# Kernel tuning notes

Measured on AMD Instinct MI355X. Metric: run time of the kernel, lower is better.

The kernel has to match this reference:

```python
import jax, jax.numpy as jnp
import numpy as np

N, E, D = 50000, 800000, 128
RESIDUAL_SCALE = 1.0
EPS = 1e-5  # torch LayerNorm default eps


def _mlp_ln(h, w1, b1, w2, b2, w3, b3, g, beta):
    # MeshGraphNets MLP: Linear -> SiLU -> Linear -> SiLU -> Linear -> LayerNorm
    h = jax.nn.silu(h @ w1 + b1)
    h = jax.nn.silu(h @ w2 + b2)
    h = h @ w3 + b3
    mu = h.mean(axis=-1, keepdims=True)
    var = ((h - mu) ** 2).mean(axis=-1, keepdims=True)
    return g * (h - mu) * jax.lax.rsqrt(var + EPS) + beta


def setup_inputs() -> dict:
    key = jax.random.key(0)
    ks = jax.random.split(key, 16)

    def lin(k, fan_in, fan_out):
        bound = 1.0 / np.sqrt(fan_in)
        kw, kb = jax.random.split(k)
        w = jax.random.uniform(kw, (fan_in, fan_out), jnp.float32, -bound, bound)
        b = jax.random.uniform(kb, (fan_out,), jnp.float32, -bound, bound)
        return w, b

    x = jax.random.normal(ks[0], (N, D), jnp.float32)
    edge_attr = jax.random.normal(ks[1], (E, D), jnp.float32)
    edge_index = jax.random.randint(ks[2], (2, E), 0, N, jnp.int32)

    ew1, eb1 = lin(ks[3], 3 * D, D)
    ew2, eb2 = lin(ks[4], D, D)
    ew3, eb3 = lin(ks[5], D, D)
    e_gamma = jnp.ones((D,), jnp.float32)
    e_beta = jnp.zeros((D,), jnp.float32)

    nw1, nb1 = lin(ks[6], 2 * D, D)
    nw2, nb2 = lin(ks[7], D, D)
    nw3, nb3 = lin(ks[8], D, D)
    n_gamma = jnp.ones((D,), jnp.float32)
    n_beta = jnp.zeros((D,), jnp.float32)

    return dict(x=x, edge_attr=edge_attr, edge_index=edge_index,
                ew1=ew1, eb1=eb1, ew2=ew2, eb2=eb2, ew3=ew3, eb3=eb3,
                e_gamma=e_gamma, e_beta=e_beta,
                nw1=nw1, nb1=nb1, nw2=nw2, nb2=nb2, nw3=nw3, nb3=nb3,
                n_gamma=n_gamma, n_beta=n_beta)


def reference(x, edge_attr, edge_index,
              ew1, eb1, ew2, eb2, ew3, eb3, e_gamma, e_beta,
              nw1, nb1, nw2, nb2, nw3, nb3, n_gamma, n_beta):
    senders, receivers = edge_index[0], edge_index[1]

    # EdgeBlock: gather endpoint node features, concat with edge_attr, MLP
    edge_in = jnp.concatenate([x[senders], x[receivers], edge_attr], axis=-1)  # [E, 3D]
    edge_mlp_out = _mlp_ln(edge_in, ew1, eb1, ew2, eb2, ew3, eb3, e_gamma, e_beta)  # [E, D]

    # NodeBlock: scatter-sum edge messages to receiver nodes, concat with x, MLP
    agg = jax.ops.segment_sum(edge_mlp_out, receivers, num_segments=N)  # [N, D]
    node_in = jnp.concatenate([x, agg], axis=-1)  # [N, 2D]
    node_mlp_out = _mlp_ln(node_in, nw1, nb1, nw2, nb2, nw3, nb3, n_gamma, n_beta)

    # Residual updates
    x_new = x + RESIDUAL_SCALE * node_mlp_out

    # PairNorm (use_pairnorm=True)
    x_centered = x_new - x_new.mean(axis=0, keepdims=True)
    rms = jnp.linalg.norm(x_centered) / jnp.sqrt(jnp.float32(x_new.shape[0])) + 1e-8
    x_new = x_centered / rms

    edge_attr_new = edge_attr + RESIDUAL_SCALE * edge_mlp_out
    return x_new, edge_attr_new
```

## Files before the change

### kernel.cpp

```cpp
#include <hip/hip_runtime.h>
#include <hip/hip_bf16.h>

#define NN 50000
#define NE 800000
#define ROWB 272

typedef unsigned short u16;
typedef unsigned int u32;
typedef __attribute__((ext_vector_type(4))) float f32x4;
typedef __attribute__((ext_vector_type(8))) short short8;


__device__ __forceinline__ u16 f2b(float f){ __hip_bfloat16 h = __float2bfloat16(f); u16 u; __builtin_memcpy(&u, &h, 2); return u; }
__device__ __forceinline__ float b2f(u16 u){ __hip_bfloat16 h; __builtin_memcpy(&h, &u, 2); return __bfloat162float(h); }
__device__ __forceinline__ float siluf(float v){
  const float e = __expf(-v);
  return v * __builtin_amdgcn_rcpf(1.f + e);
}

__device__ __forceinline__ uint4 cvt8(const float* __restrict__ s){
  const float4 a = *(const float4*)s;
  const float4 b = *(const float4*)(s + 4);
  union { u16 h[8]; uint4 q; } u;
  u.h[0]=f2b(a.x); u.h[1]=f2b(a.y); u.h[2]=f2b(a.z); u.h[3]=f2b(a.w);
  u.h[4]=f2b(b.x); u.h[5]=f2b(b.y); u.h[6]=f2b(b.z); u.h[7]=f2b(b.w);
  return u.q;
}

template<int K>
__device__ __forceinline__ void gemm128(f32x4 acc[4][2], const u16* __restrict__ sA,
                                        const u16* __restrict__ wB, int wm, int wn, int lane){
  const int l15 = lane & 15, l4 = lane >> 4;
  const u16* w0 = wB + (size_t)(wn*32 + l15)*K + l4*8;
  const u16* w1 = w0 + (size_t)16*K;
  #pragma unroll
  for (int ks = 0; ks < 4; ++ks){
    const short8 b0 = *(const short8*)(w0 + ks*32);
    const short8 b1 = *(const short8*)(w1 + ks*32);
    const int kb = ks*64 + l4*16;
    short8 a[4];
    #pragma unroll
    for (int fr = 0; fr < 4; ++fr)
      a[fr] = *(const short8*)((const char*)sA + (wm*64 + fr*16 + l15)*ROWB + kb);
    #pragma unroll
    for (int fr = 0; fr < 4; ++fr){
      acc[fr][0] = __builtin_amdgcn_mfma_f32_16x16x32_bf16(a[fr], b0, acc[fr][0], 0, 0, 0);
      acc[fr][1] = __builtin_amdgcn_mfma_f32_16x16x32_bf16(a[fr], b1, acc[fr][1], 0, 0, 0);
    }
  }
}

template<int K>
__device__ __forceinline__ void gemm64(f32x4 acc[2][4], const u16* __restrict__ sA,
                                       const u16* __restrict__ wB, int wm, int wn, int lane){
  const int l15 = lane & 15, l4 = lane >> 4;
  const u16* w0 = wB + (size_t)(wn*64 + l15)*K + l4*8;
  #pragma unroll
  for (int ks = 0; ks < 4; ++ks){
    short8 b[4];
    #pragma unroll
    for (int fc = 0; fc < 4; ++fc)
      b[fc] = *(const short8*)(w0 + (size_t)fc*16*K + ks*32);
    const int kb = ks*64 + l4*16;
    short8 a[2];
    #pragma unroll
    for (int fr = 0; fr < 2; ++fr)
      a[fr] = *(const short8*)((const char*)sA + (wm*32 + fr*16 + l15)*ROWB + kb);
    #pragma unroll
    for (int fr = 0; fr < 2; ++fr)
      #pragma unroll
      for (int fc = 0; fc < 4; ++fc)
        acc[fr][fc] = __builtin_amdgcn_mfma_f32_16x16x32_bf16(a[fr], b[fc], acc[fr][fc], 0, 0, 0);
  }
}

__device__ __forceinline__ void epilogue(const f32x4 acc[4][2], const float* __restrict__ bias,
                                         u16* __restrict__ dst, int wm, int wn, int lane, bool doSilu){
  const int l15 = lane & 15, l4 = lane >> 4;
  #pragma unroll
  for (int fc = 0; fc < 2; ++fc){
    const int col = wn*32 + fc*16 + l15;
    const float bv = bias[col];
    #pragma unroll
    for (int fr = 0; fr < 4; ++fr){
      const int rbase = wm*64 + fr*16 + l4*4;
      #pragma unroll
      for (int j = 0; j < 4; ++j){
        float v = acc[fr][fc][j] + bv;
        if (doSilu) v = siluf(v);
        *(u16*)((char*)dst + (rbase + j)*ROWB + col*2) = f2b(v);
      }
    }
  }
}

__device__ __forceinline__ void epilogue64(const f32x4 acc[2][4], const float* __restrict__ bias,
                                           u16* __restrict__ dst, int wm, int wn, int lane, bool doSilu){
  const int l15 = lane & 15, l4 = lane >> 4;
  #pragma unroll
  for (int fc = 0; fc < 4; ++fc){
    const int col = wn*64 + fc*16 + l15;
    const float bv = bias[col];
    #pragma unroll
    for (int fr = 0; fr < 2; ++fr){
      const int rbase = wm*32 + fr*16 + l4*4;
      #pragma unroll
      for (int j = 0; j < 4; ++j){
        float v = acc[fr][fc][j] + bv;
        if (doSilu) v = siluf(v);
        *(u16*)((char*)dst + (rbase + j)*ROWB + col*2) = f2b(v);
      }
    }
  }
}

__global__ __launch_bounds__(256) void prep_kernel(const float* __restrict__ w1, const float* __restrict__ w2,
                                                   const float* __restrict__ w3, const float* __restrict__ m1,
                                                   const float* __restrict__ m2, const float* __restrict__ m3,
                                                   u16* __restrict__ wt,
                                                   const float* __restrict__ x, u16* __restrict__ xB,
                                                   const int* __restrict__ eidx, int* __restrict__ cnt){
  const int i = blockIdx.x * 256 + threadIdx.x;
  if (i < 147456){
    const float* src; int K, base, off;
    if      (i < 49152)  { src = w1; K = 384; base = 0;      off = i; }
    else if (i < 65536)  { src = w2; K = 128; base = 49152;  off = i - 49152; }
    else if (i < 81920)  { src = w3; K = 128; base = 65536;  off = i - 65536; }
    else if (i < 114688) { src = m1; K = 256; base = 81920;  off = i - 81920; }
    else if (i < 131072) { src = m2; K = 128; base = 114688; off = i - 114688; }
    else                 { src = m3; K = 128; base = 131072; off = i - 131072; }
    const int k = off >> 7, n = off & 127;
    wt[base + n*K + k] = f2b(src[off]);
  }
  if (xB){
    const size_t o = (size_t)i * 8;
    *(uint4*)(xB + o) = cvt8(x + o);
  }
  atomicAdd(&cnt[eidx[NE + i]], 1);
}

__global__ __launch_bounds__(256) void scatter_kernel(const int* __restrict__ eidx, int* __restrict__ cursor,
                                                      int* __restrict__ perm){
  const int i = blockIdx.x * 256 + threadIdx.x;
  if (i < NE){
    const int pos = atomicAdd(&cursor[eidx[NE + i]], 1);
    perm[pos] = i;
  }
}

__global__ __launch_bounds__(256, 4) void scanpre_kernel(const int* __restrict__ cnt, int* __restrict__ off,
                                                         int* __restrict__ cursor,
                                                         const float* __restrict__ x, const u16* __restrict__ xB,
                                                         const u16* __restrict__ wt, u16* __restrict__ Pab){
  const int t = threadIdx.x;
  if (blockIdx.x == 0){
    __shared__ int s[256];
    const int CH = 196;
    int sum = 0;
    for (int i = 0; i < CH; ++i){
      const int idx = t*CH + i;
      if (idx < NN) sum += cnt[idx];
    }
    s[t] = sum;
    __syncthreads();
    for (int d = 1; d < 256; d <<= 1){
      int v = (t >= d) ? s[t - d] : 0;
      __syncthreads();
      s[t] += v;
      __syncthreads();
    }
    int run = s[t] - sum;
    for (int i = 0; i < CH; ++i){
      const int idx = t*CH + i;
      if (idx < NN){
        off[idx] = run;
        cursor[idx] = run;
        run += cnt[idx];
        if (idx == NN - 1) off[NN] = run;
      }
    }
    return;
  }

  __shared__ u16 sX[64*136];
  const int nBase = (blockIdx.x - 1) * 64;
  const int lane = t & 63, wid = t >> 6;
  const int wm = wid >> 1, wn = wid & 1;
  const int chunk = t & 15, r0 = t >> 4;

  #pragma unroll
  for (int p = 0; p < 4; ++p){
    const int row = r0 + p*16;
    const int node = nBase + row;
    uint4 v = {0u, 0u, 0u, 0u};
    if (node < NN){
      if (xB) v = *(const uint4*)(xB + (size_t)node*128 + chunk*8);
      else    v = cvt8(x + (size_t)node*128 + chunk*8);
    }
    *(uint4*)((char*)sX + row*ROWB + chunk*16) = v;
  }
  __syncthreads();

  const f32x4 z4 = {0.f, 0.f, 0.f, 0.f};
  const int l15 = lane & 15, l4 = lane >> 4;
  #pragma unroll
  for (int half = 0; half < 2; ++half){
    f32x4 acc[2][4];
    #pragma unroll
    for (int fr = 0; fr < 2; ++fr)
      #pragma unroll
      for (int fc = 0; fc < 4; ++fc) acc[fr][fc] = z4;
    gemm64<384>(acc, sX, wt + half*128, wm, wn, lane);
    #pragma unroll
    for (int fc = 0; fc < 4; ++fc){
      const int col = wn*64 + fc*16 + l15;
      #pragma unroll
      for (int fr = 0; fr < 2; ++fr){
        const int rbase = wm*32 + fr*16 + l4*4;
        #pragma unroll
        for (int j = 0; j < 4; ++j){
          const int node = nBase + rbase + j;
          if (node < NN) Pab[(size_t)node*256 + half*128 + col] = f2b(acc[fr][fc][j]);
        }
      }
    }
  }
}

__global__ __launch_bounds__(512, 4) void edge_kernel(
    const float* __restrict__ ea, const int* __restrict__ eidx,
    const u16* __restrict__ wt, const u16* __restrict__ Pab,
    const float* __restrict__ b1, const float* __restrict__ b2,
    const float* __restrict__ b3, const float* __restrict__ gma, const float* __restrict__ bta,
    int* __restrict__ cursor, float* __restrict__ outE, u16* __restrict__ oBuf)
{
  __shared__ u16 sA[128*136];
  __shared__ float sMeta[640];
  __shared__ int sIdx[256];
  __shared__ int sSlot[128];
  const int t = threadIdx.x;
  const size_t eBase = (size_t)blockIdx.x * 128;

  if (t < 128){
    sIdx[t] = eidx[eBase + t];
    const int r = eidx[(size_t)NE + eBase + t];
    sIdx[t + 128] = r;
    if (oBuf) sSlot[t] = atomicAdd(&cursor[r], 1);
    sMeta[t]       = b1[t];
    sMeta[t + 128] = b2[t];
    sMeta[t + 256] = b3[t];
    sMeta[t + 384] = gma[t];
    sMeta[t + 512] = bta[t];
  }
  __syncthreads();

  const int lane = t & 63, wid = t >> 6;
  const int wm = wid >> 2, wn = wid & 3;
  const int chunk = t & 15, r0 = t >> 4;
  const int l15 = lane & 15, l4 = lane >> 4;

  uint4 eaQ[4];
  #pragma unroll
  for (int p = 0; p < 4; ++p){
    const int row = r0 + p*32;
    uint4 v = cvt8(ea + ((eBase + row)*128 + chunk*8));
    eaQ[p] = v;
    *(uint4*)((char*)sA + row*ROWB + chunk*16) = v;
  }

  f32x4 acc[4][2];
  #pragma unroll
  for (int fr = 0; fr < 4; ++fr){
    #pragma unroll
    for (int j = 0; j < 4; ++j){
      const int row = wm*64 + fr*16 + l4*4 + j;
      const u16* pa = Pab + (size_t)sIdx[row]*256;
      const u16* pb = Pab + (size_t)sIdx[row + 128]*256 + 128;
      #pragma unroll
      for (int fc = 0; fc < 2; ++fc){
        const int col = wn*32 + fc*16 + l15;
        acc[fr][fc][j] = b2f(pa[col]) + b2f(pb[col]);
      }
    }
  }
  __syncthreads();

  gemm128<384>(acc, sA, wt + 256, wm, wn, lane);
  __syncthreads();
  epilogue(acc, sMeta + 0, sA, wm, wn, lane, true);
  __syncthreads();
  const f32x4 z4 = {0.f, 0.f, 0.f, 0.f};
  #pragma unroll
  for (int fr = 0; fr < 4; ++fr){ acc[fr][0] = z4; acc[fr][1] = z4; }
  gemm128<128>(acc, sA, wt + 49152, wm, wn, lane);
  __syncthreads();
  epilogue(acc, sMeta + 128, sA, wm, wn, lane, true);
  __syncthreads();
  #pragma unroll
  for (int fr = 0; fr < 4; ++fr){ acc[fr][0] = z4; acc[fr][1] = z4; }
  gemm128<128>(acc, sA, wt + 65536, wm, wn, lane);
  __syncthreads();
  epilogue(acc, sMeta + 256, sA, wm, wn, lane, false);
  __syncthreads();

  {
    #pragma unroll
    for (int p = 0; p < 4; ++p){
      const int row = r0 + p*32;
      uint4 q = *(const uint4*)((const char*)sA + row*ROWB + chunk*16);
      const u16* pu = (const u16*)&q;
      float h[8];
      #pragma unroll
      for (int j = 0; j < 8; ++j) h[j] = b2f(pu[j]);
      float s = 0.f;
      #pragma unroll
      for (int j = 0; j < 8; ++j) s += h[j];
      s += __shfl_xor(s, 1); s += __shfl_xor(s, 2); s += __shfl_xor(s, 4); s += __shfl_xor(s, 8);
      const float mu = s * (1.f/128.f);
      float ss = 0.f;
      #pragma unroll
      for (int j = 0; j < 8; ++j){ const float d = h[j] - mu; ss += d*d; }
      ss += __shfl_xor(ss, 1); ss += __shfl_xor(ss, 2); ss += __shfl_xor(ss, 4); ss += __shfl_xor(ss, 8);
      const float rs = rsqrtf(fmaxf(ss*(1.f/128.f), 0.f) + 1e-5f);
      const size_t e = eBase + row;
      const u16* ep = (const u16*)&eaQ[p];
      alignas(16) float orow[8];
      alignas(16) u16 obf[8];
      #pragma unroll
      for (int j = 0; j < 8; ++j){
        const int col = chunk*8 + j;
        const float o = sMeta[384 + col]*(h[j] - mu)*rs + sMeta[512 + col];
        orow[j] = b2f(ep[j]) + o;
        obf[j] = f2b(o);
      }
      float* dst = outE + e*128 + chunk*8;
      *(float4*)dst       = ((const float4*)orow)[0];
      *(float4*)(dst + 4) = ((const float4*)orow)[1];
      if (oBuf) *(uint4*)(oBuf + (size_t)sSlot[row]*128 + chunk*8) = *(const uint4*)obf;
    }
  }
}

__global__ __launch_bounds__(256) void agg_f_kernel(const float* __restrict__ outE, const float* __restrict__ ea,
                                                    const int* __restrict__ off, const int* __restrict__ perm,
                                                    float* __restrict__ agg){
  const int node = blockIdx.x * 4 + (threadIdx.x >> 6);
  const int lane = threadIdx.x & 63;
  if (node >= NN) return;
  const int s = off[node], e = off[node + 1];
  float a0 = 0.f, a1 = 0.f;
  for (int i = s; i < e; ++i){
    const size_t r = (size_t)perm[i] * 128;
    a0 += outE[r + lane]      - ea[r + lane];
    a1 += outE[r + 64 + lane] - ea[r + 64 + lane];
  }
  agg[(size_t)node*128 + lane]      = a0;
  agg[(size_t)node*128 + 64 + lane] = a1;
}

__global__ __launch_bounds__(256, 4) void node_kernel(
    const float* __restrict__ x, const float* __restrict__ aggF,
    const u16* __restrict__ oBuf, const int* __restrict__ off,
    const u16* __restrict__ wt,
    const float* __restrict__ b1, const float* __restrict__ b2, const float* __restrict__ b3,
    const float* __restrict__ gma, const float* __restrict__ bta,
    float* __restrict__ outX, float* __restrict__ stats)
{
  __shared__ u16 sA[64*136];
  __shared__ float sMeta[640];
  __shared__ float sCol[128];
  __shared__ float sSq;
  const int t = threadIdx.x;
  const int nBase = blockIdx.x * 64;

  if (t < 128){
    sMeta[t]       = b1[t];
    sMeta[t + 128] = b2[t];
    sMeta[t + 256] = b3[t];
    sMeta[t + 384] = gma[t];
    sMeta[t + 512] = bta[t];
    sCol[t] = 0.f;
  }
  if (t == 0) sSq = 0.f;
  __syncthreads();

  const int lane = t & 63, wid = t >> 6;
  const int wm = wid >> 1, wn = wid & 1;
  const int chunk = t & 15, r0 = t >> 4;

  const f32x4 z4 = {0.f, 0.f, 0.f, 0.f};
  f32x4 acc[2][4];
  #pragma unroll
  for (int fr = 0; fr < 2; ++fr)
    #pragma unroll
    for (int fc = 0; fc < 4; ++fc) acc[fr][fc] = z4;

  for (int kc = 0; kc < 2; ++kc){
    #pragma unroll
    for (int p = 0; p < 4; ++p){
      const int row = r0 + p*16;
      const int node = nBase + row;
      uint4 v = {0u, 0u, 0u, 0u};
      if (node < NN){
        if (kc == 0){
          v = cvt8(x + (size_t)node*128 + chunk*8);
        } else if (oBuf){
          float a[8] = {0.f,0.f,0.f,0.f,0.f,0.f,0.f,0.f};
          const int s0 = off[node], e0 = off[node + 1];
          for (int i = s0; i < e0; ++i){
            uint4 q = *(const uint4*)(oBuf + (size_t)i*128 + chunk*8);
            const u16* pu = (const u16*)&q;
            #pragma unroll
            for (int j = 0; j < 8; ++j) a[j] += b2f(pu[j]);
          }
          union { u16 h[8]; uint4 q; } u;
          #pragma unroll
          for (int j = 0; j < 8; ++j) u.h[j] = f2b(a[j]);
          v = u.q;
        } else {
          v = cvt8(aggF + (size_t)node*128 + chunk*8);
        }
      }
      *(uint4*)((char*)sA + row*ROWB + chunk*16) = v;
    }
    __syncthreads();
    gemm64<256>(acc, sA, wt + 81920 + kc*128, wm, wn, lane);
    __syncthreads();
  }
  epilogue64(acc, sMeta + 0, sA, wm, wn, lane, true);
  __syncthreads();
  #pragma unroll
  for (int fr = 0; fr < 2; ++fr)
    #pragma unroll
    for (int fc = 0; fc < 4; ++fc) acc[fr][fc] = z4;
  gemm64<128>(acc, sA, wt + 114688, wm, wn, lane);
  __syncthreads();
  epilogue64(acc, sMeta + 128, sA, wm, wn, lane, true);
  __syncthreads();
  #pragma unroll
  for (int fr = 0; fr < 2; ++fr)
    #pragma unroll
    for (int fc = 0; fc < 4; ++fc) acc[fr][fc] = z4;
  gemm64<128>(acc, sA, wt + 131072, wm, wn, lane);
  __syncthreads();
  epilogue64(acc, sMeta + 256, sA, wm, wn, lane, false);
  __syncthreads();

  {
    float lssq = 0.f;
    #pragma unroll
    for (int p = 0; p < 4; ++p){
      const int row = r0 + p*16;
      const int node = nBase + row;
      uint4 q = *(const uint4*)((const char*)sA + row*ROWB + chunk*16);
      const u16* pu = (const u16*)&q;
      float h[8];
      #pragma unroll
      for (int j = 0; j < 8; ++j) h[j] = b2f(pu[j]);
      float s = 0.f;
      #pragma unroll
      for (int j = 0; j < 8; ++j) s += h[j];
      s += __shfl_xor(s, 1); s += __shfl_xor(s, 2); s += __shfl_xor(s, 4); s += __shfl_xor(s, 8);
      const float mu = s * (1.f/128.f);
      float ss = 0.f;
      #pragma unroll
      for (int j = 0; j < 8; ++j){ const float d = h[j] - mu; ss += d*d; }
      ss += __shfl_xor(ss, 1); ss += __shfl_xor(ss, 2); ss += __shfl_xor(ss, 4); ss += __shfl_xor(ss, 8);
      const float rs = rsqrtf(fmaxf(ss*(1.f/128.f), 0.f) + 1e-5f);
      if (node < NN){
        const float* xRow = x + (size_t)node*128 + chunk*8;
        const float4 xa = *(const float4*)xRow;
        const float4 xb = *(const float4*)(xRow + 4);
        float xr[8] = {xa.x, xa.y, xa.z, xa.w, xb.x, xb.y, xb.z, xb.w};
        alignas(16) float orow[8];
        #pragma unroll
        for (int j = 0; j < 8; ++j){
          const int col = chunk*8 + j;
          const float o = sMeta[384 + col]*(h[j] - mu)*rs + sMeta[512 + col];
          const float res = xr[j] + o;
          orow[j] = res;
          atomicAdd(&sCol[col], res);
          lssq += res*res;
        }
        float* dst = outX + (size_t)node*128 + chunk*8;
        *(float4*)dst       = ((const float4*)orow)[0];
        *(float4*)(dst + 4) = ((const float4*)orow)[1];
      }
    }
    #pragma unroll
    for (int m = 1; m < 64; m <<= 1) lssq += __shfl_xor(lssq, m);
    if (lane == 0) atomicAdd(&sSq, lssq);
  }
  __syncthreads();
  if (t < 128) atomicAdd(&stats[t], sCol[t]);
  if (t == 0)  atomicAdd(&stats[128], sSq);
}

__global__ __launch_bounds__(256) void pairnorm_kernel(float* __restrict__ xOut, const float* __restrict__ stats){
  __shared__ float sMean[128];
  __shared__ float sP2[2];
  __shared__ float sInv;
  const int t = threadIdx.x;
  float m2 = 0.f;
  if (t < 128){
    const float mean = stats[t] * (1.f / (float)NN);
    sMean[t] = mean;
    m2 = mean * mean;
  }
  #pragma unroll
  for (int m = 1; m < 64; m <<= 1) m2 += __shfl_xor(m2, m);
  if ((t & 63) == 0 && t < 128) sP2[t >> 6] = m2;
  __syncthreads();
  if (t == 0){
    float ssc = stats[128] - (float)NN * (sP2[0] + sP2[1]);
    ssc = fmaxf(ssc, 0.f);
    const float rms = sqrtf(ssc * (1.f / (float)NN)) + 1e-8f;
    sInv = 1.f / rms;
  }
  __syncthreads();
  const size_t base = ((size_t)blockIdx.x * 256 + t) * 4;
  const int col = (int)(base & 127);
  float4 q = *(float4*)(xOut + base);
  const float inv = sInv;
  q.x = (q.x - sMean[col])     * inv;
  q.y = (q.y - sMean[col + 1]) * inv;
  q.z = (q.z - sMean[col + 2]) * inv;
  q.w = (q.w - sMean[col + 3]) * inv;
  *(float4*)(xOut + base) = q;
}

extern "C" void kernel_launch(void* const* d_in, const int* in_sizes, int n_in,
                              void* d_out, int out_size, void* d_ws, size_t ws_size,
                              hipStream_t stream){
  (void)in_sizes; (void)n_in; (void)out_size;
  const float* x    = (const float*)d_in[0];
  const float* ea   = (const float*)d_in[1];
  const int*   eidx = (const int*)d_in[2];
  const float* ew1  = (const float*)d_in[3];
  const float* eb1  = (const float*)d_in[4];
  const float* ew2  = (const float*)d_in[5];
  const float* eb2  = (const float*)d_in[6];
  const float* ew3  = (const float*)d_in[7];
  const float* eb3  = (const float*)d_in[8];
  const float* eg   = (const float*)d_in[9];
  const float* ebt  = (const float*)d_in[10];
  const float* nw1  = (const float*)d_in[11];
  const float* nb1  = (const float*)d_in[12];
  const float* nw2  = (const float*)d_in[13];
  const float* nb2  = (const float*)d_in[14];
  const float* nw3  = (const float*)d_in[15];
  const float* nb3  = (const float*)d_in[16];
  const float* ng   = (const float*)d_in[17];
  const float* nbt  = (const float*)d_in[18];

  u16*   wt     = (u16*)d_ws;
  float* stats  = (float*)((char*)d_ws + 294912);
  int*   cnt    = (int*)((char*)d_ws + 297216);
  int*   off    = (int*)((char*)d_ws + 497408);
  int*   cursor = (int*)((char*)d_ws + 697600);
  int*   perm   = (int*)((char*)d_ws + 897792);
  const bool useO = ws_size >= (7297792ull + (size_t)NE * 128 * 2);
  const bool useX = ws_size >= (7297792ull + (size_t)NE * 128 * 2 + (size_t)NN * 128 * 2);
  u16*   oBuf   = useO ? (u16*)((char*)d_ws + 7297792) : (u16*)nullptr;
  u16*   xB     = useX ? (u16*)((char*)d_ws + 7297792 + (size_t)NE * 128 * 2) : (u16*)nullptr;
  float* outX   = (float*)d_out;
  u16*   Pab    = (u16*)d_out;
  float* outE   = outX + (size_t)NN * 128;

  hipMemsetAsync((char*)d_ws + 294912, 0, 202496, stream);
  prep_kernel<<<3125, 256, 0, stream>>>(ew1, ew2, ew3, nw1, nw2, nw3, wt, x, xB, eidx, cnt);
  scanpre_kernel<<<783, 256, 0, stream>>>(cnt, off, cursor, x, xB, wt, Pab);
  if (!useO) scatter_kernel<<<3125, 256, 0, stream>>>(eidx, cursor, perm);
  edge_kernel<<<6250, 512, 0, stream>>>(ea, eidx, wt, Pab, eb1, eb2, eb3, eg, ebt, cursor, outE, oBuf);
  if (!useO) agg_f_kernel<<<12500, 256, 0, stream>>>(outE, ea, off, perm, outX);
  node_kernel<<<782, 256, 0, stream>>>(x, outX, oBuf, off, wt, nb1, nb2, nb3, ng, nbt, outX, stats);
  pairnorm_kernel<<<6250, 256, 0, stream>>>(outX, stats);
}
```

Before: 685.4 us.

## Give each wave its own 16-row band to drop block syncs in MLP kernels

Result: slower. 1.245 ms (+81.7%).

```diff
diff --git a/kernel.cpp b/kernel.cpp
--- a/kernel.cpp
+++ b/kernel.cpp
@@ -4,6 +4,7 @@
 #define NN 50000
 #define NE 800000
 #define ROWB 272
+#define NROWB 528
 
 typedef unsigned short u16;
 typedef unsigned int u32;
@@ -27,25 +28,31 @@
   return u.q;
 }
 
-template<int K>
-__device__ __forceinline__ void gemm128(f32x4 acc[4][2], const u16* __restrict__ sA,
-                                        const u16* __restrict__ wB, int wm, int wn, int lane){
-  const int l15 = lane & 15, l4 = lane >> 4;
-  const u16* w0 = wB + (size_t)(wn*32 + l15)*K + l4*8;
-  const u16* w1 = w0 + (size_t)16*K;
+template<int Kw>
+__device__ __forceinline__ void gemm_band(f32x4 acc[8], const char* bandA, int ldsb,
+                                          const u16* __restrict__ wB, int l15, int l4){
   #pragma unroll
   for (int ks = 0; ks < 4; ++ks){
-    const short8 b0 = *(const short8*)(w0 + ks*32);
-    const short8 b1 = *(const short8*)(w1 + ks*32);
-    const int kb = ks*64 + l4*16;
-    short8 a[4];
-    #pragma unroll
-    for (int fr = 0; fr < 4; ++fr)
-      a[fr] = *(const short8*)((const char*)sA + (wm*64 + fr*16 + l15)*ROWB + kb);
-    #pragma unroll
-    for (int fr = 0; fr < 4; ++fr){
-      acc[fr][0] = __builtin_amdgcn_mfma_f32_16x16x32_bf16(a[fr], b0, acc[fr][0], 0, 0, 0);
-      acc[fr][1] = __builtin_amdgcn_mfma_f32_16x16x32_bf16(a[fr], b1, acc[fr][1], 0, 0, 0);
+    const short8 a = *(const short8*)(bandA + l15*ldsb + ks*64 + l4*16);
+    #pragma unroll
+    for (int fc = 0; fc < 8; ++fc){
+      const short8 b = *(const short8*)(wB + (size_t)(fc*16 + l15)*Kw + ks*32 + l4*8);
+      acc[fc] = __builtin_amdgcn_mfma_f32_16x16x32_bf16(a, b, acc[fc], 0, 0, 0);
+    }
+  }
+}
+
+__device__ __forceinline__ void epi_band(const f32x4 acc[8], const float* __restrict__ bias,
+                                         char* band, int ldsb, int l15, int l4, bool doSilu){
+  #pragma unroll
+  for (int fc = 0; fc < 8; ++fc){
+    const int col = fc*16 + l15;
+    const float bv = bias[col];
+    #pragma unroll
+    for (int j = 0; j < 4; ++j){
+      float v = acc[fc][j] + bv;
+      if (doSilu) v = siluf(v);
+      *(u16*)(band + (l4*4 + j)*ldsb + col*2) = f2b(v);
     }
   }
 }
@@ -74,52 +81,13 @@
   }
 }
 
-__device__ __forceinline__ void epilogue(const f32x4 acc[4][2], const float* __restrict__ bias,
-                                         u16* __restrict__ dst, int wm, int wn, int lane, bool doSilu){
-  const int l15 = lane & 15, l4 = lane >> 4;
-  #pragma unroll
-  for (int fc = 0; fc < 2; ++fc){
-    const int col = wn*32 + fc*16 + l15;
-    const float bv = bias[col];
-    #pragma unroll
-    for (int fr = 0; fr < 4; ++fr){
-      const int rbase = wm*64 + fr*16 + l4*4;
-      #pragma unroll
-      for (int j = 0; j < 4; ++j){
-        float v = acc[fr][fc][j] + bv;
-        if (doSilu) v = siluf(v);
-        *(u16*)((char*)dst + (rbase + j)*ROWB + col*2) = f2b(v);
-      }
-    }
-  }
-}
-
-__device__ __forceinline__ void epilogue64(const f32x4 acc[2][4], const float* __restrict__ bias,
-                                           u16* __restrict__ dst, int wm, int wn, int lane, bool doSilu){
-  const int l15 = lane & 15, l4 = lane >> 4;
-  #pragma unroll
-  for (int fc = 0; fc < 4; ++fc){
-    const int col = wn*64 + fc*16 + l15;
-    const float bv = bias[col];
-    #pragma unroll
-    for (int fr = 0; fr < 2; ++fr){
-      const int rbase = wm*32 + fr*16 + l4*4;
-      #pragma unroll
-      for (int j = 0; j < 4; ++j){
-        float v = acc[fr][fc][j] + bv;
-        if (doSilu) v = siluf(v);
-        *(u16*)((char*)dst + (rbase + j)*ROWB + col*2) = f2b(v);
-      }
-    }
-  }
-}
-
 __global__ __launch_bounds__(256) void prep_kernel(const float* __restrict__ w1, const float* __restrict__ w2,
                                                    const float* __restrict__ w3, const float* __restrict__ m1,
                                                    const float* __restrict__ m2, const float* __restrict__ m3,
                                                    u16* __restrict__ wt,
                                                    const float* __restrict__ x, u16* __restrict__ xB,
-                                                   const int* __restrict__ eidx, int* __restrict__ cnt){
+                                                   const int* __restrict__ eidx, int* __restrict__ cnt,
+                                                   int* __restrict__ rank){
   const int i = blockIdx.x * 256 + threadIdx.x;
   if (i < 147456){
     const float* src; int K, base, off;
@@ -136,7 +104,7 @@
     const size_t o = (size_t)i * 8;
     *(uint4*)(xB + o) = cvt8(x + o);
   }
-  atomicAdd(&cnt[eidx[NE + i]], 1);
+  rank[i] = atomicAdd(&cnt[eidx[NE + i]], 1);
 }
 
 __global__ __launch_bounds__(256) void scatter_kernel(const int* __restrict__ eidx, int* __restrict__ cursor,
@@ -232,7 +200,8 @@
     const u16* __restrict__ wt, const u16* __restrict__ Pab,
     const float* __restrict__ b1, const float* __restrict__ b2,
     const float* __restrict__ b3, const float* __restrict__ gma, const float* __restrict__ bta,
-    int* __restrict__ cursor, float* __restrict__ outE, u16* __restrict__ oBuf)
+    const int* __restrict__ off, const int* __restrict__ rank,
+    float* __restrict__ outE, u16* __restrict__ oBuf)
 {
   __shared__ u16 sA[128*136];
   __shared__ float sMeta[640];
@@ -245,7 +214,7 @@
     sIdx[t] = eidx[eBase + t];
     const int r = eidx[(size_t)NE + eBase + t];
     sIdx[t + 128] = r;
-    if (oBuf) sSlot[t] = atomicAdd(&cursor[r], 1);
+    sSlot[t] = oBuf ? (off[r] + rank[eBase + t]) : 0;
     sMeta[t]       = b1[t];
     sMeta[t + 128] = b2[t];
     sMeta[t + 256] = b3[t];
@@ -255,89 +224,84 @@
   __syncthreads();
 
   const int lane = t & 63, wid = t >> 6;
-  const int wm = wid >> 2, wn = wid & 3;
-  const int chunk = t & 15, r0 = t >> 4;
   const int l15 = lane & 15, l4 = lane >> 4;
+  const int rowL = lane >> 2, cg = lane & 3;
+  char* band = (char*)sA + wid*16*ROWB;
+  const int rowBlk = wid*16 + rowL;
 
   uint4 eaQ[4];
-  #pragma unroll
-  for (int p = 0; p < 4; ++p){
-    const int row = r0 + p*32;
-    uint4 v = cvt8(ea + ((eBase + row)*128 + chunk*8));
-    eaQ[p] = v;
-    *(uint4*)((char*)sA + row*ROWB + chunk*16) = v;
-  }
-
-  f32x4 acc[4][2];
-  #pragma unroll
-  for (int fr = 0; fr < 4; ++fr){
+  const float* eaRow = ea + (eBase + rowBlk)*128 + cg*32;
+  #pragma unroll
+  for (int q = 0; q < 4; ++q){
+    eaQ[q] = cvt8(eaRow + q*8);
+    *(uint4*)(band + rowL*ROWB + cg*64 + q*16) = eaQ[q];
+  }
+
+  f32x4 acc[8];
+  #pragma unroll
+  for (int fc = 0; fc < 8; ++fc){
+    const int col = fc*16 + l15;
     #pragma unroll
     for (int j = 0; j < 4; ++j){
-      const int row = wm*64 + fr*16 + l4*4 + j;
-      const u16* pa = Pab + (size_t)sIdx[row]*256;
-      const u16* pb = Pab + (size_t)sIdx[row + 128]*256 + 128;
-      #pragma unroll
-      for (int fc = 0; fc < 2; ++fc){
-        const int col = wn*32 + fc*16 + l15;
-        acc[fr][fc][j] = b2f(pa[col]) + b2f(pb[col]);
-      }
-    }
-  }
-  __syncthreads();
-
-  gemm128<384>(acc, sA, wt + 256, wm, wn, lane);
-  __syncthreads();
-  epilogue(acc, sMeta + 0, sA, wm, wn, lane, true);
-  __syncthreads();
+      const int r = wid*16 + l4*4 + j;
+      acc[fc][j] = b2f(Pab[(size_t)sIdx[r]*256 + col]) +
+                   b2f(Pab[(size_t)sIdx[r + 128]*256 + 128 + col]);
+    }
+  }
+
   const f32x4 z4 = {0.f, 0.f, 0.f, 0.f};
-  #pragma unroll
-  for (int fr = 0; fr < 4; ++fr){ acc[fr][0] = z4; acc[fr][1] = z4; }
-  gemm128<128>(acc, sA, wt + 49152, wm, wn, lane);
-  __syncthreads();
-  epilogue(acc, sMeta + 128, sA, wm, wn, lane, true);
-  __syncthreads();
-  #pragma unroll
-  for (int fr = 0; fr < 4; ++fr){ acc[fr][0] = z4; acc[fr][1] = z4; }
-  gemm128<128>(acc, sA, wt + 65536, wm, wn, lane);
-  __syncthreads();
-  epilogue(acc, sMeta + 256, sA, wm, wn, lane, false);
-  __syncthreads();
-
-  {
-    #pragma unroll
-    for (int p = 0; p < 4; ++p){
-      const int row = r0 + p*32;
-      uint4 q = *(const uint4*)((const char*)sA + row*ROWB + chunk*16);
-      const u16* pu = (const u16*)&q;
-      float h[8];
-      #pragma unroll
-      for (int j = 0; j < 8; ++j) h[j] = b2f(pu[j]);
-      float s = 0.f;
-      #pragma unroll
-      for (int j = 0; j < 8; ++j) s += h[j];
-      s += __shfl_xor(s, 1); s += __shfl_xor(s, 2); s += __shfl_xor(s, 4); s += __shfl_xor(s, 8);
-      const float mu = s * (1.f/128.f);
-      float ss = 0.f;
-      #pragma unroll
-      for (int j = 0; j < 8; ++j){ const float d = h[j] - mu; ss += d*d; }
-      ss += __shfl_xor(ss, 1); ss += __shfl_xor(ss, 2); ss += __shfl_xor(ss, 4); ss += __shfl_xor(ss, 8);
-      const float rs = rsqrtf(fmaxf(ss*(1.f/128.f), 0.f) + 1e-5f);
-      const size_t e = eBase + row;
-      const u16* ep = (const u16*)&eaQ[p];
-      alignas(16) float orow[8];
-      alignas(16) u16 obf[8];
-      #pragma unroll
-      for (int j = 0; j < 8; ++j){
-        const int col = chunk*8 + j;
-        const float o = sMeta[384 + col]*(h[j] - mu)*rs + sMeta[512 + col];
-        orow[j] = b2f(ep[j]) + o;
-        obf[j] = f2b(o);
-      }
-      float* dst = outE + e*128 + chunk*8;
-      *(float4*)dst       = ((const float4*)orow)[0];
-      *(float4*)(dst + 4) = ((const float4*)orow)[1];
-      if (oBuf) *(uint4*)(oBuf + (size_t)sSlot[row]*128 + chunk*8) = *(const uint4*)obf;
-    }
+  gemm_band<384>(acc, band, ROWB, wt + 256, l15, l4);
+  epi_band(acc, sMeta + 0, band, ROWB, l15, l4, true);
+  #pragma unroll
+  for (int fc = 0; fc < 8; ++fc) acc[fc] = z4;
+  gemm_band<128>(acc, band, ROWB, wt + 49152, l15, l4);
+  epi_band(acc, sMeta + 128, band, ROWB, l15, l4, true);
+  #pragma unroll
+  for (int fc = 0; fc < 8; ++fc) acc[fc] = z4;
+  gemm_band<128>(acc, band, ROWB, wt + 65536, l15, l4);
+  epi_band(acc, sMeta + 256, band, ROWB, l15, l4, false);
+
+  const char* myRow = band + rowL*ROWB + cg*64;
+  float s = 0.f;
+  #pragma unroll
+  for (int q = 0; q < 4; ++q){
+    uint4 qv = *(const uint4*)(myRow + q*16);
+    const u16* pu = (const u16*)&qv;
+    #pragma unroll
+    for (int j = 0; j < 8; ++j) s += b2f(pu[j]);
+  }
+  s += __shfl_xor(s, 1); s += __shfl_xor(s, 2);
+  const float mu = s * (1.f/128.f);
+  float ss = 0.f;
+  #pragma unroll
+  for (int q = 0; q < 4; ++q){
+    uint4 qv = *(const uint4*)(myRow + q*16);
+    const u16* pu = (const u16*)&qv;
+    #pragma unroll
+    for (int j = 0; j < 8; ++j){ const float d = b2f(pu[j]) - mu; ss += d*d; }
+  }
+  ss += __shfl_xor(ss, 1); ss += __shfl_xor(ss, 2);
+  const float rs = rsqrtf(fmaxf(ss*(1.f/128.f), 0.f) + 1e-5f);
+  const size_t e = eBase + rowBlk;
+  float* dst = outE + e*128 + cg*32;
+  u16* od = oBuf ? (oBuf + (size_t)sSlot[rowBlk]*128 + cg*32) : (u16*)nullptr;
+  #pragma unroll
+  for (int q = 0; q < 4; ++q){
+    uint4 qv = *(const uint4*)(myRow + q*16);
+    const u16* pu = (const u16*)&qv;
+    const u16* ep = (const u16*)&eaQ[q];
+    alignas(16) float orow[8];
+    alignas(16) u16 obf[8];
+    #pragma unroll
+    for (int j = 0; j < 8; ++j){
+      const int col = cg*32 + q*8 + j;
+      const float o = sMeta[384 + col]*(b2f(pu[j]) - mu)*rs + sMeta[512 + col];
+      orow[j] = b2f(ep[j]) + o;
+      obf[j] = f2b(o);
+    }
+    *(float4*)(dst + q*8)     = ((const float4*)orow)[0];
+    *(float4*)(dst + q*8 + 4) = ((const float4*)orow)[1];
+    if (od) *(uint4*)(od + q*8) = *(const uint4*)obf;
   }
 }
 
@@ -366,7 +330,7 @@
     const float* __restrict__ gma, const float* __restrict__ bta,
     float* __restrict__ outX, float* __restrict__ stats)
 {
-  __shared__ u16 sA[64*136];
+  __shared__ u16 sN[64*264];
   __shared__ float sMeta[640];
   __shared__ float sCol[128];
   __shared__ float sSq;
@@ -385,106 +349,111 @@
   __syncthreads();
 
   const int lane = t & 63, wid = t >> 6;
-  const int wm = wid >> 1, wn = wid & 1;
-  const int chunk = t & 15, r0 = t >> 4;
-
-  const f32x4 z4 = {0.f, 0.f, 0.f, 0.f};
-  f32x4 acc[2][4];
-  #pragma unroll
-  for (int fr = 0; fr < 2; ++fr)
-    #pragma unroll
-    for (int fc = 0; fc < 4; ++fc) acc[fr][fc] = z4;
-
-  for (int kc = 0; kc < 2; ++kc){
-    #pragma unroll
-    for (int p = 0; p < 4; ++p){
-      const int row = r0 + p*16;
-      const int node = nBase + row;
-      uint4 v = {0u, 0u, 0u, 0u};
-      if (node < NN){
-        if (kc == 0){
-          v = cvt8(x + (size_t)node*128 + chunk*8);
-        } else if (oBuf){
-          float a[8] = {0.f,0.f,0.f,0.f,0.f,0.f,0.f,0.f};
-          const int s0 = off[node], e0 = off[node + 1];
-          for (int i = s0; i < e0; ++i){
-            uint4 q = *(const uint4*)(oBuf + (size_t)i*128 + chunk*8);
-            const u16* pu = (const u16*)&q;
-            #pragma unroll
-            for (int j = 0; j < 8; ++j) a[j] += b2f(pu[j]);
-          }
-          union { u16 h[8]; uint4 q; } u;
+  const int l15 = lane & 15, l4 = lane >> 4;
+  const int rowL = lane >> 2, cg = lane & 3;
+  char* band = (char*)sN + wid*16*NROWB;
+  const int node = nBase + wid*16 + rowL;
+
+  {
+    #pragma unroll
+    for (int q = 0; q < 4; ++q){
+      uint4 v = {0u,0u,0u,0u};
+      if (node < NN) v = cvt8(x + (size_t)node*128 + cg*32 + q*8);
+      *(uint4*)(band + rowL*NROWB + cg*64 + q*16) = v;
+    }
+    if (node < NN && oBuf){
+      float a32[32];
+      #pragma unroll
+      for (int j = 0; j < 32; ++j) a32[j] = 0.f;
+      const int s0 = off[node], e0 = off[node + 1];
+      for (int i = s0; i < e0; ++i){
+        const u16* src = oBuf + (size_t)i*128 + cg*32;
+        #pragma unroll
+        for (int q = 0; q < 4; ++q){
+          uint4 qv = *(const uint4*)(src + q*8);
+          const u16* pu = (const u16*)&qv;
           #pragma unroll
-          for (int j = 0; j < 8; ++j) u.h[j] = f2b(a[j]);
-          v = u.q;
-        } else {
-          v = cvt8(aggF + (size_t)node*128 + chunk*8);
+          for (int j = 0; j < 8; ++j) a32[q*8 + j] += b2f(pu[j]);
         }
       }
-      *(uint4*)((char*)sA + row*ROWB + chunk*16) = v;
-    }
-    __syncthreads();
-    gemm64<256>(acc, sA, wt + 81920 + kc*128, wm, wn, lane);
-    __syncthreads();
-  }
-  epilogue64(acc, sMeta + 0, sA, wm, wn, lane, true);
-  __syncthreads();
-  #pragma unroll
-  for (int fr = 0; fr < 2; ++fr)
-    #pragma unroll
-    for (int fc = 0; fc < 4; ++fc) acc[fr][fc] = z4;
-  gemm64<128>(acc, sA, wt + 114688, wm, wn, lane);
-  __syncthreads();
-  epilogue64(acc, sMeta + 128, sA, wm, wn, lane, true);
-  __syncthreads();
-  #pragma unroll
-  for (int fr = 0; fr < 2; ++fr)
-    #pragma unroll
-    for (int fc = 0; fc < 4; ++fc) acc[fr][fc] = z4;
-  gemm64<128>(acc, sA, wt + 131072, wm, wn, lane);
-  __syncthreads();
-  epilogue64(acc, sMeta + 256, sA, wm, wn, lane, false);
-  __syncthreads();
+      #pragma unroll
+      for (int q = 0; q < 4; ++q){
+        union { u16 h[8]; uint4 qq; } u;
+        #pragma unroll
+        for (int j = 0; j < 8; ++j) u.h[j] = f2b(a32[q*8 + j]);
+        *(uint4*)(band + rowL*NROWB + 256 + cg*64 + q*16) = u.qq;
+      }
+    } else {
+      #pragma unroll
+      for (int q = 0; q < 4; ++q){
+        uint4 v = {0u,0u,0u,0u};
+        if (node < NN) v = cvt8(aggF + (size_t)node*128 + cg*32 + q*8);
+        *(uint4*)(band + rowL*NROWB + 256 + cg*64 + q*16) = v;
+      }
+    }
+  }
+
+  const f32x4 z4 = {0.f, 0.f, 0.f, 0.f};
+  f32x4 acc[8];
+  #pragma unroll
+  for (int fc = 0; fc < 8; ++fc) acc[fc] = z4;
+  gemm_band<256>(acc, band, NROWB, wt + 81920, l15, l4);
+  gemm_band<256>(acc, band + 256, NROWB, wt + 81920 + 128, l15, l4);
+  epi_band(acc, sMeta + 0, band, NROWB, l15, l4, true);
+  #pragma unroll
+  for (int fc = 0; fc < 8; ++fc) acc[fc] = z4;
+  gemm_band<128>(acc, band, NROWB, wt + 114688, l15, l4);
+  epi_band(acc, sMeta + 128, band, NROWB, l15, l4, true);
+  #pragma unroll
+  for (int fc = 0; fc < 8; ++fc) acc[fc] = z4;
+  gemm_band<128>(acc, band, NROWB, wt + 131072, l15, l4);
+  epi_band(acc, sMeta + 256, band, NROWB, l15, l4, false);
 
   {
+    const char* myRow = band + rowL*NROWB + cg*64;
+    float s = 0.f;
+    #pragma unroll
+    for (int q = 0; q < 4; ++q){
+      uint4 qv = *(const uint4*)(myRow + q*16);
+      const u16* pu = (const u16*)&qv;
+      #pragma unroll
+      for (int j = 0; j < 8; ++j) s += b2f(pu[j]);
+    }
+    s += __shfl_xor(s, 1); s += __shfl_xor(s, 2);
+    const float mu = s * (1.f/128.f);
+    float ss = 0.f;
+    #pragma unroll
+    for (int q = 0; q < 4; ++q){
+      uint4 qv = *(const uint4*)(myRow + q*16);
+      const u16* pu = (const u16*)&qv;
+      #pragma unroll
+      for (int j = 0; j < 8; ++j){ const float d = b2f(pu[j]) - mu; ss += d*d; }
+    }
+    ss += __shfl_xor(ss, 1); ss += __shfl_xor(ss, 2);
+    const float rs = rsqrtf(fmaxf(ss*(1.f/128.f), 0.f) + 1e-5f);
     float lssq = 0.f;
-    #pragma unroll
-    for (int p = 0; p < 4; ++p){
-      const int row = r0 + p*16;
-      const int node = nBase + row;
-      uint4 q = *(const uint4*)((const char*)sA + row*ROWB + chunk*16);
-      const u16* pu = (const u16*)&q;
-      float h[8];
-      #pragma unroll
-      for (int j = 0; j < 8; ++j) h[j] = b2f(pu[j]);
-      float s = 0.f;
-      #pragma unroll
-      for (int j = 0; j < 8; ++j) s += h[j];
-      s += __shfl_xor(s, 1); s += __shfl_xor(s, 2); s += __shfl_xor(s, 4); s += __shfl_xor(s, 8);
-      const float mu = s * (1.f/128.f);
-      float ss = 0.f;
-      #pragma unroll
-      for (int j = 0; j < 8; ++j){ const float d = h[j] - mu; ss += d*d; }
-      ss += __shfl_xor(ss, 1); ss += __shfl_xor(ss, 2); ss += __shfl_xor(ss, 4); ss += __shfl_xor(ss, 8);
-      const float rs = rsqrtf(fmaxf(ss*(1.f/128.f), 0.f) + 1e-5f);
-      if (node < NN){
-        const float* xRow = x + (size_t)node*128 + chunk*8;
-        const float4 xa = *(const float4*)xRow;
-        const float4 xb = *(const float4*)(xRow + 4);
-        float xr[8] = {xa.x, xa.y, xa.z, xa.w, xb.x, xb.y, xb.z, xb.w};
+    if (node < NN){
+      float* dst = outX + (size_t)node*128 + cg*32;
+      const float* xRow = x + (size_t)node*128 + cg*32;
+      #pragma unroll
+      for (int q = 0; q < 4; ++q){
+        uint4 qv = *(const uint4*)(myRow + q*16);
+        const u16* pu = (const u16*)&qv;
+        const float4 xa = *(const float4*)(xRow + q*8);
+        const float4 xb = *(const float4*)(xRow + q*8 + 4);
+        const float xr[8] = {xa.x, xa.y, xa.z, xa.w, xb.x, xb.y, xb.z, xb.w};
         alignas(16) float orow[8];
         #pragma unroll
         for (int j = 0; j < 8; ++j){
-          const int col = chunk*8 + j;
-          const float o = sMeta[384 + col]*(h[j] - mu)*rs + sMeta[512 + col];
+          const int col = cg*32 + q*8 + j;
+          const float o = sMeta[384 + col]*(b2f(pu[j]) - mu)*rs + sMeta[512 + col];
           const float res = xr[j] + o;
           orow[j] = res;
           atomicAdd(&sCol[col], res);
           lssq += res*res;
         }
-        float* dst = outX + (size_t)node*128 + chunk*8;
-        *(float4*)dst       = ((const float4*)orow)[0];
-        *(float4*)(dst + 4) = ((const float4*)orow)[1];
+        *(float4*)(dst + q*8)     = ((const float4*)orow)[0];
+        *(float4*)(dst + q*8 + 4) = ((const float4*)orow)[1];
       }
     }
     #pragma unroll
@@ -559,6 +528,7 @@
   int*   off    = (int*)((char*)d_ws + 497408);
   int*   cursor = (int*)((char*)d_ws + 697600);
   int*   perm   = (int*)((char*)d_ws + 897792);
+  int*   rank   = (int*)((char*)d_ws + 4097792);
   const bool useO = ws_size >= (7297792ull + (size_t)NE * 128 * 2);
   const bool useX = ws_size >= (7297792ull + (size_t)NE * 128 * 2 + (size_t)NN * 128 * 2);
   u16*   oBuf   = useO ? (u16*)((char*)d_ws + 7297792) : (u16*)nullptr;
@@ -568,10 +538,10 @@
   float* outE   = outX + (size_t)NN * 128;
 
   hipMemsetAsync((char*)d_ws + 294912, 0, 202496, stream);
-  prep_kernel<<<3125, 256, 0, stream>>>(ew1, ew2, ew3, nw1, nw2, nw3, wt, x, xB, eidx, cnt);
+  prep_kernel<<<3125, 256, 0, stream>>>(ew1, ew2, ew3, nw1, nw2, nw3, wt, x, xB, eidx, cnt, rank);
   scanpre_kernel<<<783, 256, 0, stream>>>(cnt, off, cursor, x, xB, wt, Pab);
   if (!useO) scatter_kernel<<<3125, 256, 0, stream>>>(eidx, cursor, perm);
-  edge_kernel<<<6250, 512, 0, stream>>>(ea, eidx, wt, Pab, eb1, eb2, eb3, eg, ebt, cursor, outE, oBuf);
+  edge_kernel<<<6250, 512, 0, stream>>>(ea, eidx, wt, Pab, eb1, eb2, eb3, eg, ebt, off, rank, outE, oBuf);
   if (!useO) agg_f_kernel<<<12500, 256, 0, stream>>>(outE, ea, off, perm, outX);
   node_kernel<<<782, 256, 0, stream>>>(x, outX, oBuf, off, wt, nb1, nb2, nb3, ng, nbt, outX, stats);
   pairnorm_kernel<<<6250, 256, 0, stream>>>(outX, stats);
```
